# Kernel optimization log

Measured on AMD Instinct MI355X. Metric: run time of the kernel, lower is better.

Reference implementation:

```python
import jax, jax.numpy as jnp
import numpy as np

N_NODES = 50000
N_EDGES = 800000
D = 64
STEPS = 10
NEG_SLOPE = 0.2


def setup_inputs() -> dict:
    key = jax.random.key(0)
    ks = jax.random.split(key, 9)
    x = jax.random.normal(ks[0], (N_NODES, D), dtype=jnp.float32)
    edge_index_l1 = jax.random.randint(ks[1], (2, N_EDGES), 0, N_NODES, dtype=jnp.int64 if jax.config.jax_enable_x64 else jnp.int32)
    edge_index_l2 = jax.random.randint(ks[2], (2, N_EDGES), 0, N_NODES, dtype=jnp.int64 if jax.config.jax_enable_x64 else jnp.int32)
    s = 1.0 / np.sqrt(D)
    W1 = jax.random.normal(ks[3], (D, D), dtype=jnp.float32) * s
    a1_src = jax.random.normal(ks[4], (D,), dtype=jnp.float32) * s
    a1_dst = jax.random.normal(ks[5], (D,), dtype=jnp.float32) * s
    W2 = jax.random.normal(ks[6], (D, D), dtype=jnp.float32) * s
    a2_src = jax.random.normal(ks[7], (D,), dtype=jnp.float32) * s
    a2_dst = jax.random.normal(ks[8], (D,), dtype=jnp.float32) * s
    return {
        "x": x,
        "edge_index_l1": edge_index_l1,
        "edge_index_l2": edge_index_l2,
        "W1": W1, "a1_src": a1_src, "a1_dst": a1_dst,
        "W2": W2, "a2_src": a2_src, "a2_dst": a2_dst,
    }


def _gat_layer(x, src, dst, W, a_src, a_dst):
    """Single-head GATConv: out_i = sum_{j->i} softmax_i(LeakyReLU(a_s.Wx_j + a_d.Wx_i)) * Wx_j."""
    h = x @ W                                            # [N, D]
    e = jax.nn.leaky_relu((h @ a_src)[src] + (h @ a_dst)[dst], NEG_SLOPE)  # [E]
    # numerically stable segment softmax over incoming edges of each dst node
    m = jax.ops.segment_max(e, dst, num_segments=N_NODES)
    m = jax.lax.stop_gradient(jnp.where(jnp.isfinite(m), m, 0.0))
    w = jnp.exp(e - m[dst])                              # [E]
    denom = jax.ops.segment_sum(w, dst, num_segments=N_NODES)
    att = w / (denom[dst] + 1e-16)                       # [E]
    return jax.ops.segment_sum(h[src] * att[:, None], dst, num_segments=N_NODES)


def _base_operator(xt, ei1, ei2, W1, a1_src, a1_dst, W2, a2_src, a2_dst):
    h = _gat_layer(xt, ei1[0], ei1[1], W1, a1_src, a1_dst)
    h = jax.nn.elu(h)
    return _gat_layer(h, ei2[0], ei2[1], W2, a2_src, a2_dst)


def reference(x, edge_index_l1, edge_index_l2, W1, a1_src, a1_dst, W2, a2_src, a2_dst):
    ts = jnp.linspace(0.0, 1.0, STEPS, dtype=x.dtype)    # [STEPS]
    h_step = ts[1] - ts[0]                               # trapezoid-like uniform weight

    def step(acc, t):
        out = _base_operator(x * t, edge_index_l1, edge_index_l2,
                             W1, a1_src, a1_dst, W2, a2_src, a2_dst)
        return acc + out, None

    result, _ = jax.lax.scan(step, jnp.zeros_like(x), ts)
    return result * h_step
```

## Files before the change

### kernel.cpp

```cpp
#include <hip/hip_runtime.h>
#include <hip/hip_bf16.h>

#define NN 50000
#define NE 800000
#define DD 64
#define NEG 0.2f

#define RFL(x) __builtin_amdgcn_readfirstlane(x)

__global__ void k_hist(const int* __restrict__ dst1, const int* __restrict__ dst2,
                       int* __restrict__ cnt1, int* __restrict__ cnt2) {
    int e = blockIdx.x * blockDim.x + threadIdx.x;
    if (e < NE) {
        atomicAdd(&cnt1[dst1[e]], 1);
        atomicAdd(&cnt2[dst2[e]], 1);
    }
}

__global__ __launch_bounds__(1024) void k_scan(const int* __restrict__ cnt1, int* __restrict__ off1,
                                               const int* __restrict__ cnt2, int* __restrict__ off2) {
    const int* cnt = blockIdx.x ? cnt2 : cnt1;
    int* off = blockIdx.x ? off2 : off1;
    __shared__ int lds[1024];
    const int tid = threadIdx.x;
    const int CH = (NN + 1023) / 1024;
    const int base = tid * CH;
    int s = 0;
    for (int q = 0; q < CH; ++q) {
        int idx = base + q;
        if (idx < NN) s += cnt[idx];
    }
    lds[tid] = s;
    __syncthreads();
    for (int d = 1; d < 1024; d <<= 1) {
        int v = (tid >= d) ? lds[tid - d] : 0;
        __syncthreads();
        lds[tid] += v;
        __syncthreads();
    }
    int run = tid ? lds[tid - 1] : 0;
    for (int q = 0; q < CH; ++q) {
        int idx = base + q;
        if (idx < NN) { off[idx] = run; run += cnt[idx]; }
    }
    if (tid == 1023) off[NN] = lds[1023];
}

__global__ void k_scatter(const int* __restrict__ src1, const int* __restrict__ dst1,
                          const int* __restrict__ off1, int* __restrict__ fill1, int* __restrict__ csr1,
                          const int* __restrict__ src2, const int* __restrict__ dst2,
                          const int* __restrict__ off2, int* __restrict__ fill2, int* __restrict__ csr2) {
    int e = blockIdx.x * blockDim.x + threadIdx.x;
    if (e < NE) {
        int d1 = dst1[e];
        int p1 = off1[d1] + atomicAdd(&fill1[d1], 1);
        csr1[p1] = src1[e];
        int d2 = dst2[e];
        int p2 = off2[d2] + atomicAdd(&fill2[d2], 1);
        csr2[p2] = src2[e];
    }
}

__global__ __launch_bounds__(256) void k_h1(
    const float* __restrict__ x, const float* __restrict__ W1,
    const float* __restrict__ a1s, const float* __restrict__ a1d,
    float* __restrict__ H1, float* __restrict__ al1s, float* __restrict__ al1d) {
    const int lane = threadIdx.x & 63;
    const int i = blockIdx.x * 4 + (threadIdx.x >> 6);
    const float xv = x[i * DD + lane];
    float h = 0.f;
#pragma unroll
    for (int j = 0; j < DD; ++j) h = fmaf(__shfl(xv, j), W1[j * DD + lane], h);
    H1[i * DD + lane] = h;
    float ps = h * a1s[lane], pd = h * a1d[lane];
#pragma unroll
    for (int o = 32; o; o >>= 1) { ps += __shfl_xor(ps, o); pd += __shfl_xor(pd, o); }
    if (lane == 0) { al1s[i] = ps; al1d[i] = pd; }
}

__global__ void k_a2t(const float* __restrict__ W2, const float* __restrict__ a2s,
                      const float* __restrict__ a2d, float* __restrict__ t2s,
                      float* __restrict__ t2d) {
    int j = threadIdx.x & 63;
    float ss = 0.f, sd = 0.f;
#pragma unroll
    for (int d = 0; d < DD; ++d) {
        float w = W2[j * DD + d];
        ss = fmaf(w, a2s[d], ss);
        sd = fmaf(w, a2d[d], sd);
    }
    t2s[j] = ss;
    t2d[j] = sd;
}

__global__ __launch_bounds__(256) void k_l1(
    const int* __restrict__ off, const int* __restrict__ csrc,
    const float* __restrict__ al1s, const float* __restrict__ al1d,
    const float* __restrict__ H1,
    const float* __restrict__ t2s, const float* __restrict__ t2d,
    uint4* __restrict__ H2a, _Float16* __restrict__ H2b,
    float* __restrict__ al2s8, float* __restrict__ al2s9, float* __restrict__ al2d) {
    const int lane = threadIdx.x & 63;
    const int i = blockIdx.x * 4 + (threadIdx.x >> 6);
    const int p0 = RFL(off[i]);
    const int p1 = RFL(off[i + 1]);
    const float adv = al1d[i];
    float num[9], den[9];
#pragma unroll
    for (int k = 0; k < 9; ++k) { num[k] = 0.f; den[k] = 0.f; }

    auto edge = [&](int p) {
        int s = RFL(csrc[p]);
        float hv = H1[(size_t)s * DD + lane];
        float z = al1s[s] + adv;
        float c = z > 0.f ? z : NEG * z;
        float r = __expf(c * (1.f / 9.f));
        float w = r;
#pragma unroll
        for (int k = 0; k < 9; ++k) { den[k] += w; num[k] = fmaf(w, hv, num[k]); w *= r; }
    };
    int p = p0;
    for (; p + 1 < p1; p += 2) { edge(p); edge(p + 1); }
    if (p < p1) edge(p);

    const float tss = t2s[lane];
    const float tdd = t2d[lane];
    float hm[9];
#pragma unroll
    for (int k = 0; k < 9; ++k) {
        float t = (float)(k + 1) * (1.f / 9.f);
        float v = (den[k] > 0.f) ? (t * num[k] / den[k]) : 0.f;
        hm[k] = (v > 0.f) ? v : expm1f(v);
    }
#pragma unroll
    for (int k = 0; k < 9; ++k) {
        float ps = hm[k] * tss, pd = hm[k] * tdd;
#pragma unroll
        for (int o = 32; o; o >>= 1) { ps += __shfl_xor(ps, o); pd += __shfl_xor(pd, o); }
        if (lane == 0) {
            if (k < 8) al2s8[(size_t)i * 8 + k] = ps;
            else       al2s9[i] = ps;
            al2d[(size_t)i * 9 + k] = pd;
        }
    }
    union { _Float16 h[8]; uint4 u; } pk;
#pragma unroll
    for (int k = 0; k < 8; ++k) pk.h[k] = (_Float16)hm[k];
    H2a[(size_t)i * DD + lane] = pk.u;
    H2b[(size_t)i * DD + lane] = (_Float16)hm[8];
}

__global__ __launch_bounds__(256) void k_l2(
    const int* __restrict__ off, const int* __restrict__ csrc,
    const float* __restrict__ al2s8, const float* __restrict__ al2s9,
    const float* __restrict__ al2d,
    const uint4* __restrict__ H2a, const _Float16* __restrict__ H2b,
    const float* __restrict__ W2, float* __restrict__ out) {
    const int lane = threadIdx.x & 63;
    const int i = blockIdx.x * 4 + (threadIdx.x >> 6);
    const int p0 = RFL(off[i]);
    const int p1 = RFL(off[i + 1]);
    float adv[9];
#pragma unroll
    for (int k = 0; k < 9; ++k) adv[k] = al2d[(size_t)i * 9 + k];
    float num[9], den[9];
#pragma unroll
    for (int k = 0; k < 9; ++k) { num[k] = 0.f; den[k] = 0.f; }

    auto edge = [&](int p) {
        int s = RFL(csrc[p]);
        uint4 u = H2a[(size_t)s * DD + lane];
        float h9 = (float)H2b[(size_t)s * DD + lane];
        const float4* pa = (const float4*)(al2s8 + (size_t)s * 8);
        float4 A0 = pa[0], A1 = pa[1];
        float A9 = al2s9[s];
        union { uint4 v; _Float16 h[8]; } c; c.v = u;
        float as[8] = {A0.x, A0.y, A0.z, A0.w, A1.x, A1.y, A1.z, A1.w};
#pragma unroll
        for (int k = 0; k < 8; ++k) {
            float z = as[k] + adv[k];
            float lr = z > 0.f ? z : NEG * z;
            float w = __expf(lr);
            den[k] += w;
            num[k] = fmaf(w, (float)c.h[k], num[k]);
        }
        float z = A9 + adv[8];
        float lr = z > 0.f ? z : NEG * z;
        float w = __expf(lr);
        den[8] += w;
        num[8] = fmaf(w, h9, num[8]);
    };
    int p = p0;
    for (; p + 1 < p1; p += 2) { edge(p); edge(p + 1); }
    if (p < p1) edge(p);

    float vsum = 0.f;
#pragma unroll
    for (int k = 0; k < 9; ++k) vsum += (den[k] > 0.f) ? (num[k] / den[k]) : 0.f;
    float h2 = 0.f;
#pragma unroll 8
    for (int j = 0; j < DD; ++j) h2 = fmaf(__shfl(vsum, j), W2[j * DD + lane], h2);
    out[(size_t)i * DD + lane] = h2 * (1.f / 9.f);
}

extern "C" void kernel_launch(void* const* d_in, const int* in_sizes, int n_in,
                              void* d_out, int out_size, void* d_ws, size_t ws_size,
                              hipStream_t stream) {
    const float* x   = (const float*)d_in[0];
    const int*   ei1 = (const int*)d_in[1];
    const int*   ei2 = (const int*)d_in[2];
    const float* W1  = (const float*)d_in[3];
    const float* a1s = (const float*)d_in[4];
    const float* a1d = (const float*)d_in[5];
    const float* W2  = (const float*)d_in[6];
    const float* a2s = (const float*)d_in[7];
    const float* a2d = (const float*)d_in[8];
    float* out = (float*)d_out;

    const int* src1 = ei1;
    const int* dst1 = ei1 + NE;
    const int* src2 = ei2;
    const int* dst2 = ei2 + NE;

    uint4* H2a   = (uint4*)d_ws;
    float* H1    = (float*)d_ws + (size_t)NN * 256;
    float* al1s  = H1 + (size_t)NN * DD;
    float* al1d  = al1s + NN;
    float* al2s8 = al1d + NN;
    float* al2s9 = al2s8 + (size_t)NN * 8;
    float* al2d  = al2s9 + NN;
    _Float16* H2b = (_Float16*)(al2d + (size_t)NN * 9);
    int* off1 = (int*)((float*)H2b + (size_t)NN * DD / 2);
    int* off2 = off1 + (NN + 1);
    int* cnt1 = off2 + (NN + 1);
    int* cnt2 = cnt1 + NN;
    int* csr1 = cnt2 + NN;
    int* csr2 = csr1 + NE;
    float* t2s = (float*)(csr2 + NE);
    float* t2d = t2s + DD;

    const int EB = 256, EG = (NE + EB - 1) / EB;
    const int NB = NN / 4;

    hipMemsetAsync(cnt1, 0, 2 * NN * sizeof(int), stream);
    k_hist<<<EG, EB, 0, stream>>>(dst1, dst2, cnt1, cnt2);
    k_scan<<<2, 1024, 0, stream>>>(cnt1, off1, cnt2, off2);
    hipMemsetAsync(cnt1, 0, 2 * NN * sizeof(int), stream);
    k_scatter<<<EG, EB, 0, stream>>>(src1, dst1, off1, cnt1, csr1,
                                     src2, dst2, off2, cnt2, csr2);
    k_h1<<<NB, 256, 0, stream>>>(x, W1, a1s, a1d, H1, al1s, al1d);
    k_a2t<<<1, 64, 0, stream>>>(W2, a2s, a2d, t2s, t2d);

    k_l1<<<NB, 256, 0, stream>>>(off1, csr1, al1s, al1d, H1,
                                 t2s, t2d, H2a, H2b, al2s8, al2s9, al2d);
    k_l2<<<NB, 256, 0, stream>>>(off2, csr2, al2s8, al2s9, al2d, H2a, H2b, W2, out);
}
```

Measured before the change: 566.8 us.

## Compute edge attention weights lane-parallel per chunk and share via LDS

In both layer kernels, each wave now loads up to 64 incoming edges at once, one per lane, and computes their source index and exp attention weights in parallel. The results go into LDS, and the per-edge feature gather loop reads them back instead of every lane redundantly computing the exp and index work. Denominators are reduced across the wave with shuffles at the end. This removes redundant transcendental and scalar work per edge, but adds LDS traffic, a wave-local sync via waitcnt, and more LDS usage per block.

```diff
diff --git a/kernel.cpp b/kernel.cpp
--- a/kernel.cpp
+++ b/kernel.cpp
@@ -100,8 +100,10 @@
     const float* __restrict__ t2s, const float* __restrict__ t2d,
     uint4* __restrict__ H2a, _Float16* __restrict__ H2b,
     float* __restrict__ al2s8, float* __restrict__ al2s9, float* __restrict__ al2d) {
+    __shared__ int2 lsr[4][64];
     const int lane = threadIdx.x & 63;
-    const int i = blockIdx.x * 4 + (threadIdx.x >> 6);
+    const int wid = threadIdx.x >> 6;
+    const int i = blockIdx.x * 4 + wid;
     const int p0 = RFL(off[i]);
     const int p1 = RFL(off[i + 1]);
     const float adv = al1d[i];
@@ -109,19 +111,50 @@
 #pragma unroll
     for (int k = 0; k < 9; ++k) { num[k] = 0.f; den[k] = 0.f; }
 
-    auto edge = [&](int p) {
-        int s = RFL(csrc[p]);
-        float hv = H1[(size_t)s * DD + lane];
-        float z = al1s[s] + adv;
-        float c = z > 0.f ? z : NEG * z;
-        float r = __expf(c * (1.f / 9.f));
-        float w = r;
-#pragma unroll
-        for (int k = 0; k < 9; ++k) { den[k] += w; num[k] = fmaf(w, hv, num[k]); w *= r; }
-    };
-    int p = p0;
-    for (; p + 1 < p1; p += 2) { edge(p); edge(p + 1); }
-    if (p < p1) edge(p);
+    for (int base = p0; base < p1; base += 64) {
+        int m = p1 - base; if (m > 64) m = 64;
+        int sv = 0; float rv = 0.f;
+        if (lane < m) {
+            sv = csrc[base + lane];
+            float z = al1s[sv] + adv;
+            float c = z > 0.f ? z : NEG * z;
+            rv = __expf(c * (1.f / 9.f));
+        }
+        {
+            float w = rv;
+#pragma unroll
+            for (int k = 0; k < 9; ++k) { den[k] += w; w *= rv; }
+        }
+        lsr[wid][lane] = make_int2(sv, __float_as_int(rv));
+        asm volatile("s_waitcnt lgkmcnt(0)" ::: "memory");
+        int j = 0;
+        for (; j + 1 < m; j += 2) {
+            int2 e0 = lsr[wid][j];
+            int2 e1 = lsr[wid][j + 1];
+            float h0 = H1[(size_t)e0.x * DD + lane];
+            float h1v = H1[(size_t)e1.x * DD + lane];
+            float r0 = __int_as_float(e0.y), r1 = __int_as_float(e1.y);
+            float w0 = r0, w1 = r1;
+#pragma unroll
+            for (int k = 0; k < 9; ++k) {
+                num[k] = fmaf(w0, h0, num[k]);  w0 *= r0;
+                num[k] = fmaf(w1, h1v, num[k]); w1 *= r1;
+            }
+        }
+        if (j < m) {
+            int2 e0 = lsr[wid][j];
+            float h0 = H1[(size_t)e0.x * DD + lane];
+            float r0 = __int_as_float(e0.y);
+            float w0 = r0;
+#pragma unroll
+            for (int k = 0; k < 9; ++k) { num[k] = fmaf(w0, h0, num[k]); w0 *= r0; }
+        }
+    }
+#pragma unroll
+    for (int k = 0; k < 9; ++k) {
+#pragma unroll
+        for (int o = 32; o; o >>= 1) den[k] += __shfl_xor(den[k], o);
+    }
 
     const float tss = t2s[lane];
     const float tdd = t2d[lane];
@@ -156,8 +189,10 @@
     const float* __restrict__ al2d,
     const uint4* __restrict__ H2a, const _Float16* __restrict__ H2b,
     const float* __restrict__ W2, float* __restrict__ out) {
+    __shared__ float lw[4][64][12];
     const int lane = threadIdx.x & 63;
-    const int i = blockIdx.x * 4 + (threadIdx.x >> 6);
+    const int wid = threadIdx.x >> 6;
+    const int i = blockIdx.x * 4 + wid;
     const int p0 = RFL(off[i]);
     const int p1 = RFL(off[i + 1]);
     float adv[9];
@@ -167,33 +202,57 @@
 #pragma unroll
     for (int k = 0; k < 9; ++k) { num[k] = 0.f; den[k] = 0.f; }
 
-    auto edge = [&](int p) {
-        int s = RFL(csrc[p]);
-        uint4 u = H2a[(size_t)s * DD + lane];
-        float h9 = (float)H2b[(size_t)s * DD + lane];
-        const float4* pa = (const float4*)(al2s8 + (size_t)s * 8);
-        float4 A0 = pa[0], A1 = pa[1];
-        float A9 = al2s9[s];
-        union { uint4 v; _Float16 h[8]; } c; c.v = u;
-        float as[8] = {A0.x, A0.y, A0.z, A0.w, A1.x, A1.y, A1.z, A1.w};
-#pragma unroll
-        for (int k = 0; k < 8; ++k) {
-            float z = as[k] + adv[k];
-            float lr = z > 0.f ? z : NEG * z;
-            float w = __expf(lr);
-            den[k] += w;
-            num[k] = fmaf(w, (float)c.h[k], num[k]);
-        }
-        float z = A9 + adv[8];
-        float lr = z > 0.f ? z : NEG * z;
-        float w = __expf(lr);
-        den[8] += w;
-        num[8] = fmaf(w, h9, num[8]);
-    };
-    int p = p0;
-    for (; p + 1 < p1; p += 2) { edge(p); edge(p + 1); }
-    if (p < p1) edge(p);
-
+    for (int base = p0; base < p1; base += 64) {
+        int m = p1 - base; if (m > 64) m = 64;
+        int sv = 0; float wv[9];
+#pragma unroll
+        for (int k = 0; k < 9; ++k) wv[k] = 0.f;
+        if (lane < m) {
+            sv = csrc[base + lane];
+            const float4* pa = (const float4*)(al2s8 + (size_t)sv * 8);
+            float4 A0 = pa[0], A1 = pa[1];
+            float as[9] = {A0.x, A0.y, A0.z, A0.w, A1.x, A1.y, A1.z, A1.w, al2s9[sv]};
+#pragma unroll
+            for (int k = 0; k < 9; ++k) {
+                float z = as[k] + adv[k];
+                float lr = z > 0.f ? z : NEG * z;
+                wv[k] = __expf(lr);
+            }
+        }
+#pragma unroll
+        for (int k = 0; k < 9; ++k) den[k] += wv[k];
+        float* dst = &lw[wid][lane][0];
+        *(float4*)dst       = make_float4(wv[0], wv[1], wv[2], wv[3]);
+        *(float4*)(dst + 4) = make_float4(wv[4], wv[5], wv[6], wv[7]);
+        dst[8] = wv[8];
+        dst[9] = __int_as_float(sv);
+        asm volatile("s_waitcnt lgkmcnt(0)" ::: "memory");
+#pragma unroll 2
+        for (int j = 0; j < m; ++j) {
+            const float* src = &lw[wid][j][0];
+            float4 wA = *(const float4*)src;
+            float4 wB = *(const float4*)(src + 4);
+            float w8 = src[8];
+            int sj = __float_as_int(src[9]);
+            union { uint4 v; _Float16 h[8]; } c;
+            c.v = H2a[(size_t)sj * DD + lane];
+            float h9 = (float)H2b[(size_t)sj * DD + lane];
+            num[0] = fmaf(wA.x, (float)c.h[0], num[0]);
+            num[1] = fmaf(wA.y, (float)c.h[1], num[1]);
+            num[2] = fmaf(wA.z, (float)c.h[2], num[2]);
+            num[3] = fmaf(wA.w, (float)c.h[3], num[3]);
+            num[4] = fmaf(wB.x, (float)c.h[4], num[4]);
+            num[5] = fmaf(wB.y, (float)c.h[5], num[5]);
+            num[6] = fmaf(wB.z, (float)c.h[6], num[6]);
+            num[7] = fmaf(wB.w, (float)c.h[7], num[7]);
+            num[8] = fmaf(w8, h9, num[8]);
+        }
+    }
+#pragma unroll
+    for (int k = 0; k < 9; ++k) {
+#pragma unroll
+        for (int o = 32; o; o >>= 1) den[k] += __shfl_xor(den[k], o);
+    }
     float vsum = 0.f;
 #pragma unroll
     for (int k = 0; k < 9; ++k) vsum += (den[k] > 0.f) ? (num[k] / den[k]) : 0.f;
```

After: 568.9 us. Within noise of the previous version (+0.4%).
